# Kernel tuning notes

Hardware: AMD Instinct MI355X
Metric: run time of the kernel (lower is better)

## Reference

```python
import jax, jax.numpy as jnp
import numpy as np

DIM = 512
HID = 2048
E = 16
B = 8
N = 2048
THRESHOLD = 0.8
CAP_FACTOR = 2.0  # eval mode
MIN_EXPERT_CAPACITY = 4
LOSS_COEF = 0.01
CAP = max(MIN_EXPERT_CAPACITY, min(N, int(N * CAP_FACTOR / E)))  # 256


def setup_inputs() -> dict:
    key = jax.random.key(0)
    k1, k2, k3, k4 = jax.random.split(key, 4)
    x = jax.random.normal(k1, (B, N, DIM), dtype=jnp.float32)
    w_gating = jax.random.normal(k2, (DIM, E), dtype=jnp.float32)
    std1 = 1.0 / np.sqrt(HID)
    std2 = 1.0 / np.sqrt(DIM)
    w1 = jax.random.uniform(k3, (E, DIM, HID), jnp.float32, -std1, std1)
    w2 = jax.random.uniform(k4, (E, HID, DIM), jnp.float32, -std2, std2)
    return {"x": x, "w_gating": w_gating, "w1": w1, "w2": w2}


def _gate(x, w_gating):
    # raw gate probabilities [B, N, E]
    raw = jax.nn.softmax(jnp.einsum('bnd,de->bne', x, w_gating), axis=-1)
    order = jnp.argsort(-raw, axis=-1)                      # descending sort indices
    sp = jnp.take_along_axis(raw, order, axis=-1)           # sorted probs (desc)
    cum = jnp.cumsum(sp, axis=-1)
    tm = cum >= THRESHOLD
    k = jnp.argmax(tm.astype(jnp.float32), axis=-1) + 1     # dynamic k per token
    k = jnp.where(jnp.any(tm, axis=-1), k, E)
    # select top-k in sorted order, renormalize
    rank = jnp.arange(E)
    sel = (rank < k[..., None]).astype(raw.dtype)           # [B,N,E] sorted order
    selp = sp * sel
    normp = selp / jnp.sum(selp, axis=-1, keepdims=True)
    # scatter back to expert order via inverse permutation
    inv = jnp.argsort(order, axis=-1)
    mask = jnp.take_along_axis(sel, inv, axis=-1)           # expert_masks [B,N,E]
    weights = jnp.take_along_axis(normp, inv, axis=-1)      # expert_weights
    # capacity: exclusive cumsum over tokens
    pos = (jnp.cumsum(mask, axis=-2) - mask) * mask
    mask = mask * (pos < float(CAP)).astype(mask.dtype)
    pos = pos * mask
    pos_tok = jnp.sum(pos, axis=-1).astype(jnp.int32)       # [B,N] (summed across experts, as in source)
    in_cap = (pos_tok < CAP).astype(raw.dtype)
    oh = jax.nn.one_hot(pos_tok, CAP, dtype=raw.dtype) * in_cap[..., None]  # [B,N,CAP]
    dispatch = mask[..., None] * oh[..., None, :]           # [B,N,E,CAP]
    combine = (weights * mask)[..., None] * oh[..., None, :]
    density = jnp.mean(mask, axis=-2)
    density_proxy = jnp.mean(raw, axis=-2)
    loss = jnp.mean(density_proxy * density) * float(E * E)
    loss = loss + 0.0 * jnp.mean(k.astype(jnp.float32))
    return dispatch, combine, loss


def reference(x, w_gating, w1, w2):
    dispatch, combine, loss = _gate(x, w_gating)
    expert_inputs = jnp.einsum('bnd,bnec->ebcd', x, dispatch)        # [E,B,CAP,D]
    ei = expert_inputs.reshape(E, B * CAP, DIM)
    hidden = jax.nn.gelu(jnp.einsum('end,edh->enh', ei, w1), approximate=False)
    eo = jnp.einsum('enh,ehd->end', hidden, w2).reshape(E, B, CAP, DIM)
    output = jnp.einsum('ebcd,bnec->bnd', eo, combine)               # [B,N,D]
    return output, loss * LOSS_COEF
```

## Files before the change

kernel.cpp:

```cpp
#include <hip/hip_runtime.h>
#include <math.h>

#define DIMC 512
#define HIDC 2048
#define EC   16
#define BC   8
#define NC   2048
#define CAPC 256
#define BN   (BC * NC)
#define THRESH 0.8f

typedef unsigned short u16;
typedef __attribute__((ext_vector_type(8))) __bf16 bf16x8;
typedef __attribute__((ext_vector_type(4))) float f32x4;

__device__ __forceinline__ float bf2f(unsigned u) {
    union { unsigned i; float f; } v; v.i = u << 16; return v.f;
}
__device__ __forceinline__ u16 f2bf(float f) {
    union { float f; unsigned i; } v; v.f = f;
    unsigned r = v.i + 0x7fff + ((v.i >> 16) & 1);
    return (u16)(r >> 16);
}
__device__ __forceinline__ float gelu_f(float x) {
    float u = 0.7978845608028654f * (x + 0.044715f * x * x * x);
    float t = __expf(2.f * u);
    float th = 1.f - 2.f / (t + 1.f);
    return 0.5f * x * (1.f + th);
}

__global__ void init_kernel(int* __restrict__ heads, int* __restrict__ pos_tok)
{
    int i = blockIdx.x * 256 + threadIdx.x;
    if (i < EC * BC * CAPC) heads[i] = -1;
    if (i < BN) pos_tok[i] = 0;
}

__global__ __launch_bounds__(256) void gate_kernel(const float* __restrict__ x,
                                                   const float* __restrict__ wg,
                                                   float* __restrict__ raw,
                                                   float* __restrict__ weights,
                                                   float* __restrict__ maskf)
{
    __shared__ float wlds[16][516];
    __shared__ float lg[16][16];
    int t = threadIdx.x;
    int tok16 = t >> 4, e = t & 15;
    int token = blockIdx.x * 16 + tok16;

    {
        const float4* wg4 = (const float4*)wg;
#pragma unroll
        for (int j = 0; j < 8; ++j) {
            int idx4 = j * 256 + t;
            float4 v = wg4[idx4];
            int d  = idx4 >> 2;
            int e0 = (idx4 & 3) * 4;
            wlds[e0 + 0][d] = v.x;
            wlds[e0 + 1][d] = v.y;
            wlds[e0 + 2][d] = v.z;
            wlds[e0 + 3][d] = v.w;
        }
    }
    __syncthreads();

    const float4* xr = (const float4*)(x + (size_t)token * DIMC);
    const float4* wl = (const float4*)&wlds[e][0];
    float a0 = 0.f, a1 = 0.f, a2 = 0.f, a3 = 0.f;
#pragma unroll 4
    for (int i = 0; i < 128; i += 4) {
        float4 xa = xr[i], xb = xr[i+1], xc = xr[i+2], xd = xr[i+3];
        float4 wa = wl[i], wb = wl[i+1], wc = wl[i+2], wd = wl[i+3];
        a0 = fmaf(xa.w, wa.w, fmaf(xa.z, wa.z, fmaf(xa.y, wa.y, fmaf(xa.x, wa.x, a0))));
        a1 = fmaf(xb.w, wb.w, fmaf(xb.z, wb.z, fmaf(xb.y, wb.y, fmaf(xb.x, wb.x, a1))));
        a2 = fmaf(xc.w, wc.w, fmaf(xc.z, wc.z, fmaf(xc.y, wc.y, fmaf(xc.x, wc.x, a2))));
        a3 = fmaf(xd.w, wd.w, fmaf(xd.z, wd.z, fmaf(xd.y, wd.y, fmaf(xd.x, wd.x, a3))));
    }
    float logit = (a0 + a1) + (a2 + a3);

    float m = logit;
#pragma unroll
    for (int off = 8; off >= 1; off >>= 1) m = fmaxf(m, __shfl_xor(m, off, 16));
    float p = expf(logit - m);
    float s = p;
#pragma unroll
    for (int off = 8; off >= 1; off >>= 1) s += __shfl_xor(s, off, 16);
    p = p / s;

    int rank = 0;
    float cum = p;
#pragma unroll
    for (int j = 1; j < 16; ++j) {
        float op = __shfl_xor(p, j, 16);
        int oidx = e ^ j;
        bool ahead = (op > p) || (op == p && oidx < e);
        if (ahead) { rank++; cum += op; }
    }
    bool tm = (cum >= THRESH);
    int kr = tm ? rank : (EC - 1);
#pragma unroll
    for (int off = 8; off >= 1; off >>= 1) kr = min(kr, __shfl_xor(kr, off, 16));
    bool sel = (rank <= kr);

    float dsel = sel ? p : 0.f;
    float denom = dsel;
#pragma unroll
    for (int off = 8; off >= 1; off >>= 1) denom += __shfl_xor(denom, off, 16);
    float w = sel ? (p / denom) : 0.f;

    size_t o = (size_t)token * EC + e;
    raw[o]     = p;
    weights[o] = w;
    maskf[o]   = sel ? 1.f : 0.f;
    (void)lg;
}

__global__ __launch_bounds__(64) void capacity_kernel(const float* __restrict__ raw,
                                                      float* __restrict__ maskf,
                                                      int* __restrict__ pos,
                                                      int* __restrict__ pos_tok,
                                                      float* __restrict__ density,
                                                      float* __restrict__ proxy)
{
    int t = blockIdx.x;
    int b = t / EC, e = t % EC;
    int lane = threadIdx.x;

    size_t idx = ((size_t)b * NC + lane) * EC + e;
    const size_t step = (size_t)64 * EC;
    float mv = maskf[idx];
    float rv = raw[idx];

    int count = 0;
    float rsum = 0.f;
    for (int n0 = 0; n0 < NC; n0 += 64) {
        float mn = 0.f, rn = 0.f;
        if (n0 + 64 < NC) { mn = maskf[idx + step]; rn = raw[idx + step]; }

        rsum += rv;
        unsigned long long bal = __ballot(mv != 0.f);
        int below = __popcll(bal & ((1ull << lane) - 1ull));
        int pval = 0;
        if (mv != 0.f) {
            pval = count + below;
            if (pval >= CAPC) { maskf[idx] = 0.f; pval = 0; }
            else if (pval > 0) atomicAdd(&pos_tok[b * NC + n0 + lane], pval);
        }
        pos[idx] = pval;
        count += __popcll(bal);

        idx += step; mv = mn; rv = rn;
    }
#pragma unroll
    for (int off = 32; off >= 1; off >>= 1) rsum += __shfl_xor(rsum, off);
    if (lane == 0) {
        int admitted = count < CAPC ? count : CAPC;
        density[t] = (float)admitted / (float)NC;
        proxy[t]   = rsum / (float)NC;
    }
}

__global__ __launch_bounds__(256) void build_kernel(const float* __restrict__ maskf,
                                                    const int* __restrict__ pos,
                                                    const int* __restrict__ pos_tok,
                                                    int* __restrict__ heads,
                                                    int* __restrict__ nxt,
                                                    int* __restrict__ node_tok)
{
    int id = blockIdx.x * 256 + threadIdx.x;
    int token = id >> 4, e = id & 15;
    if (maskf[id] == 0.f) return;
    int c = pos_tok[token];
    if (c >= CAPC) return;
    int b = token >> 11;
    int slot = (e * BC + b) * CAPC + c;
    int node = (e * BC + b) * CAPC + pos[id];
    node_tok[node] = token;
    nxt[node] = atomicExch(&heads[slot], node);
}

__global__ __launch_bounds__(256) void gather_ei_kernel(const float* __restrict__ x,
                                                        const int* __restrict__ heads,
                                                        const int* __restrict__ nxt,
                                                        const int* __restrict__ node_tok,
                                                        u16* __restrict__ ei)
{
    int slot = blockIdx.x * 4 + (threadIdx.x >> 6);
    int lane = threadIdx.x & 63;
    float a[8] = {0,0,0,0,0,0,0,0};
    int node = heads[slot];
    while (node >= 0) {
        const float4* xr = (const float4*)(x + (size_t)node_tok[node] * DIMC) + lane * 2;
        float4 v0 = xr[0], v1 = xr[1];
        a[0]+=v0.x; a[1]+=v0.y; a[2]+=v0.z; a[3]+=v0.w;
        a[4]+=v1.x; a[5]+=v1.y; a[6]+=v1.z; a[7]+=v1.w;
        node = nxt[node];
    }
    uint4 v;
    v.x = (unsigned)f2bf(a[0]) | ((unsigned)f2bf(a[1]) << 16);
    v.y = (unsigned)f2bf(a[2]) | ((unsigned)f2bf(a[3]) << 16);
    v.z = (unsigned)f2bf(a[4]) | ((unsigned)f2bf(a[5]) << 16);
    v.w = (unsigned)f2bf(a[6]) | ((unsigned)f2bf(a[7]) << 16);
    *(uint4*)(ei + (size_t)slot * DIMC + lane * 8) = v;
}

__global__ __launch_bounds__(256) void transpose_cvt_kernel(const float* __restrict__ in,
                                                            u16* __restrict__ out,
                                                            int R, int C)
{
    __shared__ float tile[64][65];
    size_t eoff = (size_t)blockIdx.z * R * C;
    int c0 = blockIdx.x * 64, r0 = blockIdx.y * 64;
    int tid = threadIdx.x;
    int rr = tid >> 4;
    int cc = (tid & 15) * 4;
#pragma unroll
    for (int i = 0; i < 4; ++i) {
        float4 v = *(const float4*)(in + eoff + (size_t)(r0 + rr + 16 * i) * C + c0 + cc);
        tile[rr + 16 * i][cc + 0] = v.x;
        tile[rr + 16 * i][cc + 1] = v.y;
        tile[rr + 16 * i][cc + 2] = v.z;
        tile[rr + 16 * i][cc + 3] = v.w;
    }
    __syncthreads();
    int c = tid >> 2;
    int r8 = (tid & 3) * 16;
    u16 buf[16];
#pragma unroll
    for (int j = 0; j < 16; ++j) buf[j] = f2bf(tile[r8 + j][c]);
    u16* op = out + eoff + (size_t)(c0 + c) * R + r0 + r8;
    *(uint4*)(op)     = *(uint4*)&buf[0];
    *(uint4*)(op + 8) = *(uint4*)&buf[8];
}

__device__ __forceinline__ void async_cp16(const u16* g, u16* l) {
    __builtin_amdgcn_global_load_lds(
        (const __attribute__((address_space(1))) unsigned*)g,
        (__attribute__((address_space(3))) unsigned*)l, 16, 0, 0);
}

#define GFENCE() asm volatile("" ::: "memory")
#define BAR() do { GFENCE(); __builtin_amdgcn_s_barrier(); GFENCE(); } while (0)

template<int GELU>
__global__ __launch_bounds__(512, 2) void gemm256_kernel(
    const u16* __restrict__ A, const u16* __restrict__ Bt, u16* __restrict__ C,
    int M, int N, int K, long sA, long sB, long sC)
{
    __shared__ __align__(16) u16 lds[2][2][2][8192];
    const int e = blockIdx.z;
    const int bm = blockIdx.y * 256, bn = blockIdx.x * 256;
    const int t = threadIdx.x, lane = t & 63, w = t >> 6;
    const int wm = w & 1;
    const int wn = w >> 1;
    const int bh = wn >> 1;
    const int q = lane >> 4, m16 = lane & 15;

    const u16* g[2][2][2];
    int lofs[2];
#pragma unroll
    for (int j = 0; j < 2; ++j) {
        int l = j * 512 + t, r = l >> 3, c = (l & 7) ^ (r & 7);
        lofs[j] = l * 8;
        g[0][0][j] = A  + (size_t)e * sA + (size_t)(bm + r) * K + c * 8;
        g[0][1][j] = A  + (size_t)e * sA + (size_t)(bm + 128 + r) * K + c * 8;
        g[1][0][j] = Bt + (size_t)e * sB + (size_t)(bn + r) * K + c * 8;
        g[1][1][j] = Bt + (size_t)e * sB + (size_t)(bn + 128 + r) * K + c * 8;
    }

    int aro[8], bro[4];
#pragma unroll
    for (int mt = 0; mt < 8; ++mt) {
        int r = mt * 16 + m16;
        aro[mt] = r * 64 + (q ^ (r & 7)) * 8;
    }
#pragma unroll
    for (int nt = 0; nt < 4; ++nt) {
        int r = (wn & 1) * 64 + nt * 16 + m16;
        bro[nt] = r * 64 + (q ^ (r & 7)) * 8;
    }

    auto STAGE = [&](int buf, int op, int half) {
#pragma unroll
        for (int j = 0; j < 2; ++j) {
            async_cp16(g[op][half][j], &lds[buf][op][half][lofs[j]]);
            g[op][half][j] += 64;
        }
    };

    const int nk = K >> 6;
    STAGE(0, 1, 0); STAGE(0, 1, 1);
    STAGE(0, 0, 0); STAGE(0, 0, 1);
    if (nk > 1) {
        STAGE(1, 1, 0); STAGE(1, 1, 1);
        asm volatile("s_waitcnt vmcnt(4)" ::: "memory");
    } else {
        asm volatile("s_waitcnt vmcnt(0)" ::: "memory");
    }
    BAR();

    f32x4 acc[8][4] = {};
    for (int ti = 0; ti < nk; ++ti) {
        const int cur = ti & 1, nx = cur ^ 1;
        const u16* lA = &lds[cur][0][wm][0];
        const u16* lB = &lds[cur][1][bh][0];
        bf16x8 a0[4][2], a1[4][2], b01[2][2], b23[2][2];

#pragma unroll
        for (int mt = 0; mt < 4; ++mt)
#pragma unroll
            for (int kk = 0; kk < 2; ++kk)
                a0[mt][kk] = *(const bf16x8*)&lA[aro[mt] ^ (kk * 32)];
#pragma unroll
        for (int nt = 0; nt < 2; ++nt)
#pragma unroll
            for (int kk = 0; kk < 2; ++kk)
                b01[nt][kk] = *(const bf16x8*)&lB[bro[nt] ^ (kk * 32)];
        if (ti + 1 < nk) STAGE(nx, 0, 0);
        BAR();
        asm volatile("s_waitcnt lgkmcnt(0)" ::: "memory");
        __builtin_amdgcn_s_setprio(1);
#pragma unroll
        for (int mt = 0; mt < 4; ++mt)
#pragma unroll
            for (int nt = 0; nt < 2; ++nt)
#pragma unroll
                for (int kk = 0; kk < 2; ++kk)
                    acc[mt][nt] = __builtin_amdgcn_mfma_f32_16x16x32_bf16(
                        a0[mt][kk], b01[nt][kk], acc[mt][nt], 0, 0, 0);
        __builtin_amdgcn_s_setprio(0);
        BAR();

#pragma unroll
        for (int nt = 0; nt < 2; ++nt)
#pragma unroll
            for (int kk = 0; kk < 2; ++kk)
                b23[nt][kk] = *(const bf16x8*)&lB[bro[2 + nt] ^ (kk * 32)];
        if (ti + 1 < nk) STAGE(nx, 0, 1);
        BAR();
        asm volatile("s_waitcnt lgkmcnt(0)" ::: "memory");
        __builtin_amdgcn_s_setprio(1);
#pragma unroll
        for (int mt = 0; mt < 4; ++mt)
#pragma unroll
            for (int nt = 0; nt < 2; ++nt)
#pragma unroll
                for (int kk = 0; kk < 2; ++kk)
                    acc[mt][2 + nt] = __builtin_amdgcn_mfma_f32_16x16x32_bf16(
                        a0[mt][kk], b23[nt][kk], acc[mt][2 + nt], 0, 0, 0);
        __builtin_amdgcn_s_setprio(0);
        BAR();

#pragma unroll
        for (int mt = 0; mt < 4; ++mt)
#pragma unroll
            for (int kk = 0; kk < 2; ++kk)
                a1[mt][kk] = *(const bf16x8*)&lA[aro[4 + mt] ^ (kk * 32)];
        if (ti + 2 < nk) STAGE(cur, 1, 0);
        BAR();
        asm volatile("s_waitcnt lgkmcnt(0)" ::: "memory");
        __builtin_amdgcn_s_setprio(1);
#pragma unroll
        for (int mt = 0; mt < 4; ++mt)
#pragma unroll
            for (int nt = 0; nt < 2; ++nt)
#pragma unroll
                for (int kk = 0; kk < 2; ++kk)
                    acc[4 + mt][2 + nt] = __builtin_amdgcn_mfma_f32_16x16x32_bf16(
                        a1[mt][kk], b23[nt][kk], acc[4 + mt][2 + nt], 0, 0, 0);
        __builtin_amdgcn_s_setprio(0);
        BAR();

        if (ti + 2 < nk) STAGE(cur, 1, 1);
        BAR();
        __builtin_amdgcn_s_setprio(1);
#pragma unroll
        for (int mt = 0; mt < 4; ++mt)
#pragma unroll
            for (int nt = 0; nt < 2; ++nt)
#pragma unroll
                for (int kk = 0; kk < 2; ++kk)
                    acc[4 + mt][nt] = __builtin_amdgcn_mfma_f32_16x16x32_bf16(
                        a1[mt][kk], b01[nt][kk], acc[4 + mt][nt], 0, 0, 0);
        __builtin_amdgcn_s_setprio(0);
        if (ti + 1 < nk) {
            if (ti + 2 < nk) asm volatile("s_waitcnt vmcnt(4)" ::: "memory");
            else             asm volatile("s_waitcnt vmcnt(0)" ::: "memory");
        }
        BAR();
    }

    const size_t cbase = (size_t)e * sC;
#pragma unroll
    for (int mt = 0; mt < 8; ++mt)
#pragma unroll
        for (int nt = 0; nt < 4; ++nt)
#pragma unroll
            for (int r2 = 0; r2 < 4; ++r2) {
                int row = bm + wm * 128 + mt * 16 + q * 4 + r2;
                int col = bn + wn * 64 + nt * 16 + m16;
                float v = acc[mt][nt][r2];
                if (GELU) v = gelu_f(v);
                C[cbase + (size_t)row * N + col] = f2bf(v);
            }
}

__global__ __launch_bounds__(256) void combine_kernel(const u16* __restrict__ eo,
                                                      const float* __restrict__ weights,
                                                      const float* __restrict__ maskf,
                                                      const int* __restrict__ pos_tok,
                                                      float* __restrict__ out)
{
    int token = blockIdx.x;
    int tid   = threadIdx.x;
    int b = token >> 11;
    int c = pos_tok[token];
    float a0 = 0.f, a1 = 0.f;
    if (c < CAPC) {
        const float* wr = weights + (size_t)token * EC;
        const float* mr = maskf   + (size_t)token * EC;
#pragma unroll
        for (int e = 0; e < EC; ++e) {
            float wm = wr[e] * mr[e];
            if (wm != 0.f) {
                const u16* src = eo + (((size_t)e * BC + b) * CAPC + c) * DIMC;
                unsigned u = *(const unsigned*)(src + 2 * tid);
                a0 += wm * bf2f(u & 0xffffu);
                a1 += wm * bf2f(u >> 16);
            }
        }
    }
    *(float2*)(out + (size_t)token * DIMC + 2 * tid) = make_float2(a0, a1);
}

__global__ void loss_kernel(const float* __restrict__ density,
                            const float* __restrict__ proxy,
                            float* __restrict__ out_loss)
{
    __shared__ float sh[BC * EC];
    int t = threadIdx.x;
    sh[t] = density[t] * proxy[t];
    __syncthreads();
    for (int s2 = (BC * EC) / 2; s2 >= 1; s2 >>= 1) {
        if (t < s2) sh[t] += sh[t + s2];
        __syncthreads();
    }
    if (t == 0)
        out_loss[0] = sh[0] * ((float)(EC * EC) / (float)(BC * EC)) * 0.01f;
}

extern "C" void kernel_launch(void* const* d_in, const int* in_sizes, int n_in,
                              void* d_out, int out_size, void* d_ws, size_t ws_size,
                              hipStream_t stream)
{
    const float* x  = (const float*)d_in[0];
    const float* wg = (const float*)d_in[1];
    const float* w1 = (const float*)d_in[2];
    const float* w2 = (const float*)d_in[3];
    float* out = (float*)d_out;

    char* ws = (char*)d_ws;
    size_t off = 0;
    auto alloc = [&](size_t bytes) -> void* {
        void* p = ws + off;
        off = (off + bytes + 255) & ~(size_t)255;
        return p;
    };
    float* raw      = (float*)alloc((size_t)BN * EC * 4);
    float* weights  = (float*)alloc((size_t)BN * EC * 4);
    float* maskf    = (float*)alloc((size_t)BN * EC * 4);
    int*   pos      = (int*)  alloc((size_t)BN * EC * 4);
    int*   pos_tok  = (int*)  alloc((size_t)BN * 4);
    int*   heads    = (int*)  alloc((size_t)EC * BC * CAPC * 4);
    int*   nxt      = (int*)  alloc((size_t)EC * BC * CAPC * 4);
    int*   node_tok = (int*)  alloc((size_t)EC * BC * CAPC * 4);
    float* density  = (float*)alloc(BC * EC * 4);
    float* proxy    = (float*)alloc(BC * EC * 4);
    u16*   ei_bf    = (u16*)alloc((size_t)EC * BC * CAPC * DIMC * 2);
    u16*   w1t      = (u16*)alloc((size_t)EC * DIMC * HIDC * 2);
    u16*   w2t      = (u16*)alloc((size_t)EC * HIDC * DIMC * 2);
    u16*   eo_bf    = (u16*)alloc((size_t)EC * BC * CAPC * DIMC * 2);
    size_t hid_full = (size_t)EC * BC * CAPC * HIDC * 2;
    int ngroups = (ws_size - off >= hid_full) ? 1 : 2;
    int EG = EC / ngroups;
    u16* hidden = (u16*)alloc((size_t)EG * BC * CAPC * HIDC * 2);

    (void)in_sizes; (void)n_in; (void)out_size;

    init_kernel<<<(EC * BC * CAPC + 255) / 256, 256, 0, stream>>>(heads, pos_tok);
    transpose_cvt_kernel<<<dim3(HIDC / 64, DIMC / 64, EC), 256, 0, stream>>>(w1, w1t, DIMC, HIDC);
    transpose_cvt_kernel<<<dim3(DIMC / 64, HIDC / 64, EC), 256, 0, stream>>>(w2, w2t, HIDC, DIMC);

    gate_kernel<<<BN / 16, 256, 0, stream>>>(x, wg, raw, weights, maskf);
    capacity_kernel<<<BC * EC, 64, 0, stream>>>(raw, maskf, pos, pos_tok, density, proxy);
    build_kernel<<<BN * EC / 256, 256, 0, stream>>>(maskf, pos, pos_tok, heads, nxt, node_tok);
    gather_ei_kernel<<<EC * BC * CAPC / 4, 256, 0, stream>>>(x, heads, nxt, node_tok, ei_bf);

    for (int g = 0; g < ngroups; ++g) {
        const u16* Ag  = ei_bf + (size_t)g * EG * BC * CAPC * DIMC;
        const u16* B1g = w1t   + (size_t)g * EG * DIMC * HIDC;
        gemm256_kernel<1><<<dim3(HIDC / 256, (BC * CAPC) / 256, EG), 512, 0, stream>>>(
            Ag, B1g, hidden, BC * CAPC, HIDC, DIMC,
            (long)BC * CAPC * DIMC, (long)HIDC * DIMC, (long)BC * CAPC * HIDC);
        const u16* B2g = w2t + (size_t)g * EG * HIDC * DIMC;
        u16* Eg = eo_bf + (size_t)g * EG * BC * CAPC * DIMC;
        gemm256_kernel<0><<<dim3(DIMC / 256, (BC * CAPC) / 256, EG), 512, 0, stream>>>(
            hidden, B2g, Eg, BC * CAPC, DIMC, HIDC,
            (long)BC * CAPC * HIDC, (long)DIMC * HIDC, (long)BC * CAPC * DIMC);
    }

    combine_kernel<<<BN, 256, 0, stream>>>(eo_bf, weights, maskf, pos_tok, out);
    loss_kernel<<<1, BC * EC, 0, stream>>>(density, proxy, out + (size_t)BN * DIMC);
}
```

Measured before the change: 492.6 us.

## Add 128x256-tile FFN2 GEMM and merge weight transpose launches

Adds a dedicated second-expert-GEMM kernel with 128x256 output tiles, 16 accumulators per wave and launch bounds allowing two blocks per CU. This doubles the grid for the K=2048, N=512 GEMM, which previously had only 2x8x16 blocks of 256x256. It also merges the two weight transpose/convert launches into one kernel that dispatches on block index. The smaller tile gives less operand reuse per block in exchange for better occupancy and wave balance.

```diff
diff --git a/kernel.cpp b/kernel.cpp
--- a/kernel.cpp
+++ b/kernel.cpp
@@ -204,13 +204,26 @@
     *(uint4*)(ei + (size_t)slot * DIMC + lane * 8) = v;
 }
 
-__global__ __launch_bounds__(256) void transpose_cvt_kernel(const float* __restrict__ in,
-                                                            u16* __restrict__ out,
-                                                            int R, int C)
+__global__ __launch_bounds__(256) void transpose_cvt_all_kernel(const float* __restrict__ w1,
+                                                                const float* __restrict__ w2,
+                                                                u16* __restrict__ w1t,
+                                                                u16* __restrict__ w2t)
 {
     __shared__ float tile[64][65];
-    size_t eoff = (size_t)blockIdx.z * R * C;
-    int c0 = blockIdx.x * 64, r0 = blockIdx.y * 64;
+    int bid = blockIdx.x;
+    const float* in; u16* out; int R, C, bx, by, e;
+    if (bid < 4096) {
+        e = bid >> 8; int r = bid & 255;
+        bx = r & 31; by = r >> 5;
+        in = w1; out = w1t; R = DIMC; C = HIDC;
+    } else {
+        bid -= 4096;
+        e = bid >> 8; int r = bid & 255;
+        bx = r & 7;  by = r >> 3;
+        in = w2; out = w2t; R = HIDC; C = DIMC;
+    }
+    size_t eoff = (size_t)e * R * C;
+    int c0 = bx * 64, r0 = by * 64;
     int tid = threadIdx.x;
     int rr = tid >> 4;
     int cc = (tid & 15) * 4;
@@ -402,6 +415,163 @@
                 float v = acc[mt][nt][r2];
                 if (GELU) v = gelu_f(v);
                 C[cbase + (size_t)row * N + col] = f2bf(v);
+            }
+}
+
+__global__ __launch_bounds__(512, 2) void gemm_ffn2_kernel(
+    const u16* __restrict__ A, const u16* __restrict__ Bt, u16* __restrict__ C,
+    int N, int K, long sA, long sB, long sC)
+{
+    __shared__ __align__(16) u16 lds[2][3][8192];
+    const int e = blockIdx.z;
+    const int bm = blockIdx.y * 128, bn = blockIdx.x * 256;
+    const int t = threadIdx.x, lane = t & 63, w = t >> 6;
+    const int wm = w & 1, wn = w >> 1;
+    const int bh = wn >> 1;
+    const int q = lane >> 4, m16 = lane & 15;
+
+    const u16* gA[2]; const u16* gB[2][2];
+    int lofs[2];
+#pragma unroll
+    for (int j = 0; j < 2; ++j) {
+        int l = j * 512 + t, r = l >> 3, c = (l & 7) ^ (r & 7);
+        lofs[j] = l * 8;
+        gA[j]    = A  + (size_t)e * sA + (size_t)(bm + r) * K + c * 8;
+        gB[0][j] = Bt + (size_t)e * sB + (size_t)(bn + r) * K + c * 8;
+        gB[1][j] = Bt + (size_t)e * sB + (size_t)(bn + 128 + r) * K + c * 8;
+    }
+
+    int aro[4], bro[4];
+#pragma unroll
+    for (int mt = 0; mt < 4; ++mt) {
+        int r = wm * 64 + mt * 16 + m16;
+        aro[mt] = r * 64 + (q ^ (r & 7)) * 8;
+    }
+#pragma unroll
+    for (int nt = 0; nt < 4; ++nt) {
+        int r = (wn & 1) * 64 + nt * 16 + m16;
+        bro[nt] = r * 64 + (q ^ (r & 7)) * 8;
+    }
+
+    auto STAGE_A = [&](int buf) {
+#pragma unroll
+        for (int j = 0; j < 2; ++j) { async_cp16(gA[j], &lds[buf][0][lofs[j]]); gA[j] += 64; }
+    };
+    auto STAGE_B = [&](int buf, int half) {
+#pragma unroll
+        for (int j = 0; j < 2; ++j) { async_cp16(gB[half][j], &lds[buf][1 + half][lofs[j]]); gB[half][j] += 64; }
+    };
+
+    const int nk = K >> 6;
+    STAGE_A(0); STAGE_B(0, 0); STAGE_B(0, 1);
+    if (nk > 1) {
+        STAGE_B(1, 0); STAGE_B(1, 1);
+        asm volatile("s_waitcnt vmcnt(4)" ::: "memory");
+    } else {
+        asm volatile("s_waitcnt vmcnt(0)" ::: "memory");
+    }
+    BAR();
+
+    f32x4 acc[4][4] = {};
+    for (int ti = 0; ti < nk; ++ti) {
+        const int cur = ti & 1, nx = cur ^ 1;
+        const u16* lA = &lds[cur][0][0];
+        const u16* lB = &lds[cur][1 + bh][0];
+        bf16x8 a01[2][2], a23[2][2], b01[2][2], b23[2][2];
+
+#pragma unroll
+        for (int mt = 0; mt < 2; ++mt)
+#pragma unroll
+            for (int kk = 0; kk < 2; ++kk)
+                a01[mt][kk] = *(const bf16x8*)&lA[aro[mt] ^ (kk * 32)];
+#pragma unroll
+        for (int nt = 0; nt < 2; ++nt)
+#pragma unroll
+            for (int kk = 0; kk < 2; ++kk)
+                b01[nt][kk] = *(const bf16x8*)&lB[bro[nt] ^ (kk * 32)];
+        if (ti + 1 < nk) STAGE_A(nx);
+        BAR();
+        asm volatile("s_waitcnt lgkmcnt(0)" ::: "memory");
+        __builtin_amdgcn_s_setprio(1);
+#pragma unroll
+        for (int mt = 0; mt < 2; ++mt)
+#pragma unroll
+            for (int nt = 0; nt < 2; ++nt)
+#pragma unroll
+                for (int kk = 0; kk < 2; ++kk)
+                    acc[mt][nt] = __builtin_amdgcn_mfma_f32_16x16x32_bf16(
+                        a01[mt][kk], b01[nt][kk], acc[mt][nt], 0, 0, 0);
+        __builtin_amdgcn_s_setprio(0);
+        BAR();
+
+#pragma unroll
+        for (int nt = 0; nt < 2; ++nt)
+#pragma unroll
+            for (int kk = 0; kk < 2; ++kk)
+                b23[nt][kk] = *(const bf16x8*)&lB[bro[2 + nt] ^ (kk * 32)];
+        BAR();
+        asm volatile("s_waitcnt lgkmcnt(0)" ::: "memory");
+        __builtin_amdgcn_s_setprio(1);
+#pragma unroll
+        for (int mt = 0; mt < 2; ++mt)
+#pragma unroll
+            for (int nt = 0; nt < 2; ++nt)
+#pragma unroll
+                for (int kk = 0; kk < 2; ++kk)
+                    acc[mt][2 + nt] = __builtin_amdgcn_mfma_f32_16x16x32_bf16(
+                        a01[mt][kk], b23[nt][kk], acc[mt][2 + nt], 0, 0, 0);
+        __builtin_amdgcn_s_setprio(0);
+        BAR();
+
+#pragma unroll
+        for (int mt = 0; mt < 2; ++mt)
+#pragma unroll
+            for (int kk = 0; kk < 2; ++kk)
+                a23[mt][kk] = *(const bf16x8*)&lA[aro[2 + mt] ^ (kk * 32)];
+        if (ti + 2 < nk) STAGE_B(cur, 0);
+        BAR();
+        asm volatile("s_waitcnt lgkmcnt(0)" ::: "memory");
+        __builtin_amdgcn_s_setprio(1);
+#pragma unroll
+        for (int mt = 0; mt < 2; ++mt)
+#pragma unroll
+            for (int nt = 0; nt < 2; ++nt)
+#pragma unroll
+                for (int kk = 0; kk < 2; ++kk)
+                    acc[2 + mt][2 + nt] = __builtin_amdgcn_mfma_f32_16x16x32_bf16(
+                        a23[mt][kk], b23[nt][kk], acc[2 + mt][2 + nt], 0, 0, 0);
+        __builtin_amdgcn_s_setprio(0);
+        BAR();
+
+        if (ti + 2 < nk) STAGE_B(cur, 1);
+        BAR();
+        __builtin_amdgcn_s_setprio(1);
+#pragma unroll
+        for (int mt = 0; mt < 2; ++mt)
+#pragma unroll
+            for (int nt = 0; nt < 2; ++nt)
+#pragma unroll
+                for (int kk = 0; kk < 2; ++kk)
+                    acc[2 + mt][nt] = __builtin_amdgcn_mfma_f32_16x16x32_bf16(
+                        a23[mt][kk], b01[nt][kk], acc[2 + mt][nt], 0, 0, 0);
+        __builtin_amdgcn_s_setprio(0);
+        if (ti + 1 < nk) {
+            if (ti + 2 < nk) asm volatile("s_waitcnt vmcnt(4)" ::: "memory");
+            else             asm volatile("s_waitcnt vmcnt(0)" ::: "memory");
+        }
+        BAR();
+    }
+
+    const size_t cbase = (size_t)e * sC;
+#pragma unroll
+    for (int mt = 0; mt < 4; ++mt)
+#pragma unroll
+        for (int nt = 0; nt < 4; ++nt)
+#pragma unroll
+            for (int r2 = 0; r2 < 4; ++r2) {
+                int row = bm + wm * 64 + mt * 16 + q * 4 + r2;
+                int col = bn + wn * 64 + nt * 16 + m16;
+                C[cbase + (size_t)row * N + col] = f2bf(acc[mt][nt][r2]);
             }
 }
 
@@ -488,8 +658,7 @@
     (void)in_sizes; (void)n_in; (void)out_size;
 
     init_kernel<<<(EC * BC * CAPC + 255) / 256, 256, 0, stream>>>(heads, pos_tok);
-    transpose_cvt_kernel<<<dim3(HIDC / 64, DIMC / 64, EC), 256, 0, stream>>>(w1, w1t, DIMC, HIDC);
-    transpose_cvt_kernel<<<dim3(DIMC / 64, HIDC / 64, EC), 256, 0, stream>>>(w2, w2t, HIDC, DIMC);
+    transpose_cvt_all_kernel<<<8192, 256, 0, stream>>>(w1, w2, w1t, w2t);
 
     gate_kernel<<<BN / 16, 256, 0, stream>>>(x, wg, raw, weights, maskf);
     capacity_kernel<<<BC * EC, 64, 0, stream>>>(raw, maskf, pos, pos_tok, density, proxy);
@@ -504,8 +673,8 @@
             (long)BC * CAPC * DIMC, (long)HIDC * DIMC, (long)BC * CAPC * HIDC);
         const u16* B2g = w2t + (size_t)g * EG * HIDC * DIMC;
         u16* Eg = eo_bf + (size_t)g * EG * BC * CAPC * DIMC;
-        gemm256_kernel<0><<<dim3(DIMC / 256, (BC * CAPC) / 256, EG), 512, 0, stream>>>(
-            hidden, B2g, Eg, BC * CAPC, DIMC, HIDC,
+        gemm_ffn2_kernel<<<dim3(DIMC / 256, (BC * CAPC) / 128, EG), 512, 0, stream>>>(
+            hidden, B2g, Eg, DIMC, HIDC,
             (long)BC * CAPC * HIDC, (long)DIMC * HIDC, (long)BC * CAPC * DIMC);
     }
 
```

Measured after the change: 451.9 us. 8.3% less time.
